# Performance work log

Measured on AMD Instinct MI355X. Metric: run time of the kernel, lower is better.

Reference implementation:

```python
import jax, jax.numpy as jnp
import numpy as np

HEADS = 8


def setup_inputs() -> dict:
    key = jax.random.key(0)
    k1, k2, k3, k4, k5, k6 = jax.random.split(key, 6)
    B, S, E = 2, 2048, 512
    D = E // HEADS
    return {
        "values": jax.random.normal(k1, (B, S, E), dtype=jnp.float32),
        "keys": jax.random.normal(k2, (B, S, E), dtype=jnp.float32),
        "queries": jax.random.normal(k3, (B, S, E), dtype=jnp.float32),
        "mask": jax.random.randint(k4, (B, 1, 1, S), 0, 2, dtype=jnp.int32),
        "W_v": jax.random.normal(k5, (D, D), dtype=jnp.float32) * (1.0 / np.sqrt(D)),
        "W_o": jax.random.normal(k6, (E, E), dtype=jnp.float32) * (1.0 / np.sqrt(E)),
        "b_o": jnp.zeros((E,), dtype=jnp.float32),
    }


def reference(values, keys, queries, mask, W_v, W_o, b_o):
    B, S, E = queries.shape
    H = HEADS
    D = E // H
    # reshape to (b, s, h, d) and apply the SAME W_v linear to v, k, q
    # (faithful to the original, which calls self.values on all three)
    v = jnp.einsum('bshd,ed->bshe', values.reshape(B, -1, H, D), W_v)
    k = jnp.einsum('bshd,ed->bshe', keys.reshape(B, -1, H, D), W_v)
    q = jnp.einsum('bshd,ed->bshe', queries.reshape(B, -1, H, D), W_v)
    # unscaled attention scores (original has no 1/sqrt(d))
    energy = jnp.einsum('bqhd,bkhd->bhqk', q, k)  # (b, h, q, k)
    energy = jnp.where(mask == 0, -jnp.inf, energy)
    attn = jax.nn.softmax(energy, axis=3)
    out = jnp.einsum('bhqk,bkhd->bqhd', attn, v)  # (b, q, h, d)
    out = out.reshape(B, S, E)
    return out @ W_o.T + b_o
```

## Files before the change

kernel.cpp:

```cpp
#include <hip/hip_runtime.h>


#define B_ 2
#define S_ 2048
#define E_ 512
#define H_ 8
#define D_ 64

#define LOG2E 1.4426950408889634f
#define KEEP_BIAS (-92.332483f)

typedef unsigned short ushort_t;
typedef __attribute__((ext_vector_type(8))) short short8;
typedef __attribute__((ext_vector_type(8))) _Float16 half8;
typedef __attribute__((ext_vector_type(4))) float f32x4;

__device__ __forceinline__ ushort_t f2bs(float x) {
    union { float f; unsigned int u; } a; a.f = x;
    unsigned int u = a.u;
    u += 0x7fffu + ((u >> 16) & 1u);
    return (ushort_t)(u >> 16);
}
__device__ __forceinline__ ushort_t f2hs(float x) {
    _Float16 h = (_Float16)x;
    ushort_t u; __builtin_memcpy(&u, &h, 2);
    return u;
}

__global__ void __launch_bounds__(256) proj_mfma(
    const float* __restrict__ quer, const float* __restrict__ keys,
    const float* __restrict__ vals, const float* __restrict__ Wv,
    const float* __restrict__ Wo,
    ushort_t* __restrict__ qf, ushort_t* __restrict__ kf,
    ushort_t* __restrict__ vt, ushort_t* __restrict__ Wob)
{
    __shared__ ushort_t As[64 * 72];
    __shared__ ushort_t Bs[64 * 72];
    const int tens = blockIdx.y;
    const int bx = blockIdx.x;
    const int t = threadIdx.x;

    if (tens == 3) {
        if (bx < 128) {
            int g = (bx * 256 + t) * 8;
            float4 f0 = *(const float4*)(Wo + g);
            float4 f1 = *(const float4*)(Wo + g + 4);
            ushort_t tmp[8] = {f2bs(f0.x), f2bs(f0.y), f2bs(f0.z), f2bs(f0.w),
                               f2bs(f1.x), f2bs(f1.y), f2bs(f1.z), f2bs(f1.w)};
            *(uint4*)&Wob[g] = *(uint4*)tmp;
        }
        return;
    }

    const float* src = tens == 0 ? quer : (tens == 1 ? keys : vals);
    const int st = bx & 31, bh = bx >> 5;
    const int b = bh >> 3, h = bh & 7;
    const int s0 = st * 64;

    {
        int e = t >> 2, dg = (t & 3) * 16;
        const float4* g = (const float4*)(Wv + e * 64 + dg);
        ushort_t tmp[16];
        #pragma unroll
        for (int q = 0; q < 4; ++q) {
            float4 f = g[q];
            tmp[q * 4 + 0] = f2hs(f.x); tmp[q * 4 + 1] = f2hs(f.y);
            tmp[q * 4 + 2] = f2hs(f.z); tmp[q * 4 + 3] = f2hs(f.w);
        }
        *(uint4*)&Bs[e * 72 + dg]     = *(uint4*)tmp;
        *(uint4*)&Bs[e * 72 + dg + 8] = *(uint4*)(tmp + 8);
    }
    {
        int row = t >> 2, cg = (t & 3) * 16;
        const float4* g = (const float4*)(src + ((size_t)b * S_ + s0 + row) * 512 + h * 64 + cg);
        ushort_t tmp[16];
        #pragma unroll
        for (int q = 0; q < 4; ++q) {
            float4 f = g[q];
            tmp[q * 4 + 0] = f2hs(f.x); tmp[q * 4 + 1] = f2hs(f.y);
            tmp[q * 4 + 2] = f2hs(f.z); tmp[q * 4 + 3] = f2hs(f.w);
        }
        *(uint4*)&As[row * 72 + cg]     = *(uint4*)tmp;
        *(uint4*)&As[row * 72 + cg + 8] = *(uint4*)(tmp + 8);
    }
    __syncthreads();

    const int w = t >> 6, lm = t & 15, quad = (t >> 4) & 3;
    f32x4 acc[4];
    #pragma unroll
    for (int nt = 0; nt < 4; ++nt) acc[nt] = (f32x4){0.f, 0.f, 0.f, 0.f};

    __builtin_amdgcn_s_setprio(1);
    #pragma unroll
    for (int kk = 0; kk < 2; ++kk) {
        half8 a = *(const half8*)&As[(w * 16 + lm) * 72 + kk * 32 + quad * 8];
        #pragma unroll
        for (int nt = 0; nt < 4; ++nt) {
            half8 bb = *(const half8*)&Bs[(nt * 16 + lm) * 72 + kk * 32 + quad * 8];
            acc[nt] = __builtin_amdgcn_mfma_f32_16x16x32_f16(a, bb, acc[nt], 0, 0, 0);
        }
    }
    __builtin_amdgcn_s_setprio(0);

    if (tens < 2) {
        ushort_t* dst = tens == 0 ? qf : kf;
        const float sc = tens == 0 ? LOG2E : 1.0f;
        #pragma unroll
        for (int nt = 0; nt < 4; ++nt) {
            #pragma unroll
            for (int r = 0; r < 4; ++r) {
                size_t addr = ((size_t)bh * S_ + s0 + w * 16 + quad * 4 + r) * 64 + nt * 16 + lm;
                dst[addr] = f2hs(acc[nt][r] * sc);
            }
        }
    } else {
        #pragma unroll
        for (int nt = 0; nt < 4; ++nt) {
            unsigned int p0 = (unsigned int)f2bs(acc[nt][0]) | ((unsigned int)f2bs(acc[nt][1]) << 16);
            unsigned int p1 = (unsigned int)f2bs(acc[nt][2]) | ((unsigned int)f2bs(acc[nt][3]) << 16);
            uint2 pk; pk.x = p0; pk.y = p1;
            size_t addr = ((size_t)bh * 64 + nt * 16 + lm) * S_ + s0 + w * 16 + quad * 4;
            *(uint2*)&vt[addr] = pk;
        }
    }
}

__global__ void __launch_bounds__(512, 4) attn_mfma(
    const ushort_t* __restrict__ qf, const ushort_t* __restrict__ kf,
    const ushort_t* __restrict__ vt, const int* __restrict__ mask,
    ushort_t* __restrict__ ctx)
{
    __shared__ ushort_t Ks[2][64 * 72];
    __shared__ ushort_t Vt[2][64 * 72];
    __shared__ ushort_t Ps[8 * 16 * 72];
    __shared__ float    mb[2][64];

    const int bx = blockIdx.x;
    const int qt = bx & 31;
    const int bh = bx >> 5;
    const int b  = bh >> 3;
    const int t  = threadIdx.x;
    const int w  = t >> 6;
    const int wq = w & 3;
    const int ws = w >> 2;
    const int lm = t & 15, quad = (t >> 4) & 3;
    const int q0 = qt * 64;
    const int wbase = w * 16 * 72;

    const int srow = t >> 3;
    const int scg  = (t & 7) * 8;
    const size_t kgbase = ((size_t)bh * S_ + srow) * 64 + scg;
    const size_t vgbase = ((size_t)bh * 64 + srow) * S_ + scg;

    half8 aq[2];
    {
        size_t qrow = ((size_t)bh * S_ + q0 + wq * 16 + lm) * 64 + quad * 8;
        aq[0] = *(const half8*)&qf[qrow];
        aq[1] = *(const half8*)&qf[qrow + 32];
    }
    short8 ones;
    #pragma unroll
    for (int j = 0; j < 8; ++j) ones[j] = (short)0x3F80;

    f32x4 acc[4];
    #pragma unroll
    for (int nt = 0; nt < 4; ++nt) acc[nt] = (f32x4){0.f, 0.f, 0.f, 0.f};
    f32x4 acc_l = (f32x4){0.f, 0.f, 0.f, 0.f};

    {
        *(uint4*)&Ks[0][srow * 72 + scg] = *(const uint4*)&kf[kgbase];
        *(uint4*)&Ks[1][srow * 72 + scg] = *(const uint4*)&kf[kgbase + 4096];
        *(uint4*)&Vt[0][srow * 72 + scg] = *(const uint4*)&vt[vgbase];
        *(uint4*)&Vt[1][srow * 72 + scg] = *(const uint4*)&vt[vgbase + 64];
        if (t < 128) mb[t >> 6][t & 63] = mask[b * S_ + t] ? KEEP_BIAS : -1e30f;
    }
    __syncthreads();

    for (int is = 0; is < S_ / 128; ++is) {
        const bool pf = (is + 1) < (S_ / 128);

        uint4 pk0, pk1, pv0, pv1; int mnx = 0;
        if (pf) {
            size_t ko = kgbase + (size_t)(2 * (is + 1)) * 4096;
            pk0 = *(const uint4*)&kf[ko];
            pk1 = *(const uint4*)&kf[ko + 4096];
            size_t vo = vgbase + (size_t)(2 * (is + 1)) * 64;
            pv0 = *(const uint4*)&vt[vo];
            pv1 = *(const uint4*)&vt[vo + 64];
            if (t < 128) mnx = mask[b * S_ + (2 * (is + 1)) * 64 + t];
        }

        const ushort_t* Kc = Ks[ws];
        const ushort_t* Vc = Vt[ws];

        #pragma unroll
        for (int nt = 0; nt < 4; ++nt) {
            f32x4 s = *(const f32x4*)&mb[ws][nt * 16 + quad * 4];
            __builtin_amdgcn_s_setprio(1);
            #pragma unroll
            for (int kk = 0; kk < 2; ++kk) {
                half8 ak = *(const half8*)&Kc[(nt * 16 + lm) * 72 + kk * 32 + quad * 8];
                s = __builtin_amdgcn_mfma_f32_16x16x32_f16(ak, aq[kk], s, 0, 0, 0);
            }
            __builtin_amdgcn_s_setprio(0);
            float p0 = __builtin_amdgcn_exp2f(s[0]);
            float p1 = __builtin_amdgcn_exp2f(s[1]);
            float p2 = __builtin_amdgcn_exp2f(s[2]);
            float p3 = __builtin_amdgcn_exp2f(s[3]);
            uint2 pkd;
            pkd.x = (unsigned int)f2bs(p0) | ((unsigned int)f2bs(p1) << 16);
            pkd.y = (unsigned int)f2bs(p2) | ((unsigned int)f2bs(p3) << 16);
            *(uint2*)&Ps[wbase + lm * 72 + nt * 16 + quad * 4] = pkd;
        }

        __builtin_amdgcn_s_setprio(1);
        #pragma unroll
        for (int kk = 0; kk < 2; ++kk) {
            short8 ap = *(const short8*)&Ps[wbase + lm * 72 + kk * 32 + quad * 8];
            #pragma unroll
            for (int nt = 0; nt < 4; ++nt) {
                short8 bv = *(const short8*)&Vc[(nt * 16 + lm) * 72 + kk * 32 + quad * 8];
                acc[nt] = __builtin_amdgcn_mfma_f32_16x16x32_bf16(ap, bv, acc[nt], 0, 0, 0);
            }
            acc_l = __builtin_amdgcn_mfma_f32_16x16x32_bf16(ap, ones, acc_l, 0, 0, 0);
        }
        __builtin_amdgcn_s_setprio(0);

        __syncthreads();
        if (pf) {
            *(uint4*)&Ks[0][srow * 72 + scg] = pk0;
            *(uint4*)&Ks[1][srow * 72 + scg] = pk1;
            *(uint4*)&Vt[0][srow * 72 + scg] = pv0;
            *(uint4*)&Vt[1][srow * 72 + scg] = pv1;
            if (t < 128) mb[t >> 6][t & 63] = mnx ? KEEP_BIAS : -1e30f;
            __syncthreads();
        }
    }

    float* cf = (float*)Ps;
    const int lane = t & 63;
    __syncthreads();
    if (ws == 1) {
        const int base = (wq * 64 + lane) * 18;
        #pragma unroll
        for (int nt = 0; nt < 4; ++nt) {
            #pragma unroll
            for (int r = 0; r < 4; r += 2) {
                float2 v2; v2.x = acc[nt][r]; v2.y = acc[nt][r + 1];
                *(float2*)&cf[base + nt * 4 + r] = v2;
            }
        }
    }
    __syncthreads();
    if (ws == 0) {
        const int base = (wq * 64 + lane) * 18;
        #pragma unroll
        for (int nt = 0; nt < 4; ++nt) {
            #pragma unroll
            for (int r = 0; r < 4; ++r) acc[nt][r] += cf[base + nt * 4 + r];
        }
    }
    __syncthreads();
    if (ws == 1) {
        const int base = (wq * 64 + lane) * 5;
        #pragma unroll
        for (int r = 0; r < 4; ++r) cf[base + r] = acc_l[r];
    }
    __syncthreads();

    if (ws == 0) {
        const int base = (wq * 64 + lane) * 5;
        #pragma unroll
        for (int r = 0; r < 4; ++r) acc_l[r] += cf[base + r];
        const int h = bh & 7;
        #pragma unroll
        for (int r = 0; r < 4; ++r) {
            float inv = 1.f / acc_l[r];
            int s = q0 + wq * 16 + quad * 4 + r;
            #pragma unroll
            for (int nt = 0; nt < 4; ++nt) {
                int d = nt * 16 + lm;
                ctx[((size_t)b * S_ + s) * E_ + h * D_ + d] = f2bs(acc[nt][r] * inv);
            }
        }
    }
}

__global__ void __launch_bounds__(512, 4) outproj_mfma(
    const ushort_t* __restrict__ ctx, const ushort_t* __restrict__ Wob,
    const float* __restrict__ bo, float* __restrict__ out)
{
    __shared__ ushort_t sm[4][64 * 72];
    const int m0 = blockIdx.x * 64, n0 = blockIdx.y * 64;
    const int t = threadIdx.x;
    const int w = t >> 6, wq = w & 3, wk = w >> 2;
    const int lm = t & 15, quad = (t >> 4) & 3;
    const int srow = t >> 3, scg = (t & 7) * 8;

    const size_t abase = (size_t)(m0 + srow) * E_ + scg;
    const size_t bbase = (size_t)(n0 + srow) * E_ + scg;

    f32x4 acc[4];
    #pragma unroll
    for (int nt = 0; nt < 4; ++nt) acc[nt] = (f32x4){0.f, 0.f, 0.f, 0.f};

    *(uint4*)&sm[0][srow * 72 + scg] = *(const uint4*)&ctx[abase];
    *(uint4*)&sm[1][srow * 72 + scg] = *(const uint4*)&ctx[abase + 256];
    *(uint4*)&sm[2][srow * 72 + scg] = *(const uint4*)&Wob[bbase];
    *(uint4*)&sm[3][srow * 72 + scg] = *(const uint4*)&Wob[bbase + 256];
    __syncthreads();

    const ushort_t* Ac = sm[wk];
    const ushort_t* Bc = sm[2 + wk];

    for (int is = 0; is < 4; ++is) {
        const bool pf = is < 3;
        uint4 pa0, pa1, pb0, pb1;
        if (pf) {
            pa0 = *(const uint4*)&ctx[abase + (size_t)(is + 1) * 64];
            pa1 = *(const uint4*)&ctx[abase + 256 + (size_t)(is + 1) * 64];
            pb0 = *(const uint4*)&Wob[bbase + (size_t)(is + 1) * 64];
            pb1 = *(const uint4*)&Wob[bbase + 256 + (size_t)(is + 1) * 64];
        }

        __builtin_amdgcn_s_setprio(1);
        #pragma unroll
        for (int kk = 0; kk < 2; ++kk) {
            short8 a = *(const short8*)&Ac[(wq * 16 + lm) * 72 + kk * 32 + quad * 8];
            #pragma unroll
            for (int nt = 0; nt < 4; ++nt) {
                short8 bb = *(const short8*)&Bc[(nt * 16 + lm) * 72 + kk * 32 + quad * 8];
                acc[nt] = __builtin_amdgcn_mfma_f32_16x16x32_bf16(a, bb, acc[nt], 0, 0, 0);
            }
        }
        __builtin_amdgcn_s_setprio(0);

        __syncthreads();
        if (pf) {
            *(uint4*)&sm[0][srow * 72 + scg] = pa0;
            *(uint4*)&sm[1][srow * 72 + scg] = pa1;
            *(uint4*)&sm[2][srow * 72 + scg] = pb0;
            *(uint4*)&sm[3][srow * 72 + scg] = pb1;
            __syncthreads();
        }
    }

    float* cf = (float*)sm;
    const int lane = t & 63;
    if (wk == 1) {
        const int base = (wq * 64 + lane) * 18;
        #pragma unroll
        for (int nt = 0; nt < 4; ++nt) {
            #pragma unroll
            for (int r = 0; r < 4; r += 2) {
                float2 v2; v2.x = acc[nt][r]; v2.y = acc[nt][r + 1];
                *(float2*)&cf[base + nt * 4 + r] = v2;
            }
        }
    }
    __syncthreads();
    if (wk == 0) {
        const int base = (wq * 64 + lane) * 18;
        #pragma unroll
        for (int nt = 0; nt < 4; ++nt) {
            float bias = bo[n0 + nt * 16 + lm];
            #pragma unroll
            for (int r = 0; r < 4; ++r) {
                int m = m0 + wq * 16 + quad * 4 + r;
                out[(size_t)m * E_ + n0 + nt * 16 + lm] =
                    acc[nt][r] + cf[base + nt * 4 + r] + bias;
            }
        }
    }
}

extern "C" void kernel_launch(void* const* d_in, const int* in_sizes, int n_in,
                              void* d_out, int out_size, void* d_ws, size_t ws_size,
                              hipStream_t stream) {
    const float* vals = (const float*)d_in[0];
    const float* keys = (const float*)d_in[1];
    const float* quer = (const float*)d_in[2];
    const int*   mask = (const int*)d_in[3];
    const float* Wv   = (const float*)d_in[4];
    const float* Wo   = (const float*)d_in[5];
    const float* bo   = (const float*)d_in[6];
    float* out = (float*)d_out;

    const size_t N = (size_t)B_ * H_ * S_ * D_;
    ushort_t* ws  = (ushort_t*)d_ws;
    ushort_t* qf  = ws;
    ushort_t* kf  = ws + N;
    ushort_t* vt  = ws + 2 * N;
    ushort_t* ctx = ws + 3 * N;
    ushort_t* Wob = ws + 4 * N;

    proj_mfma<<<dim3(B_ * H_ * (S_ / 64), 4), 256, 0, stream>>>(
        quer, keys, vals, Wv, Wo, qf, kf, vt, Wob);
    attn_mfma<<<B_ * H_ * (S_ / 64), 512, 0, stream>>>(qf, kf, vt, mask, ctx);
    outproj_mfma<<<dim3((B_ * S_) / 64, E_ / 64), 512, 0, stream>>>(ctx, Wob, bo, out);
}
```

Before: 124.6 us.

## Load V fragments directly from global, double-buffer K in LDS, swizzle block order

The attention kernel stops staging V^T through shared memory and has each lane load its MFMA B-operand fragments straight from global memory every iteration. K and the mask bias are now double-buffered in LDS, which cuts the loop to one barrier per iteration instead of two. The block index is remapped so neighbouring blocks spread across heads. The aim is to reduce LDS traffic and synchronisation, in exchange for less-coalesced global V loads whose latency sits on the critical path and for more LDS used by the K double buffer.

New measurement: 158.7 us. 27.4% more time.

```diff
diff --git a/kernel.cpp b/kernel.cpp
--- a/kernel.cpp
+++ b/kernel.cpp
@@ -130,12 +130,12 @@
     const ushort_t* __restrict__ vt, const int* __restrict__ mask,
     ushort_t* __restrict__ ctx)
 {
-    __shared__ ushort_t Ks[2][64 * 72];
-    __shared__ ushort_t Vt[2][64 * 72];
+    __shared__ ushort_t Ks[2][2][64 * 72];
     __shared__ ushort_t Ps[8 * 16 * 72];
-    __shared__ float    mb[2][64];
-
-    const int bx = blockIdx.x;
+    __shared__ float    mb[2][2][64];
+
+    const int bx0 = blockIdx.x;
+    const int bx = (bx0 & 7) * 64 + (bx0 >> 3);
     const int qt = bx & 31;
     const int bh = bx >> 5;
     const int b  = bh >> 3;
@@ -150,7 +150,8 @@
     const int srow = t >> 3;
     const int scg  = (t & 7) * 8;
     const size_t kgbase = ((size_t)bh * S_ + srow) * 64 + scg;
-    const size_t vgbase = ((size_t)bh * 64 + srow) * S_ + scg;
+
+    const ushort_t* vB = vt + ((size_t)bh * 64 + lm) * S_ + quad * 8;
 
     half8 aq[2];
     {
@@ -168,34 +169,39 @@
     f32x4 acc_l = (f32x4){0.f, 0.f, 0.f, 0.f};
 
     {
-        *(uint4*)&Ks[0][srow * 72 + scg] = *(const uint4*)&kf[kgbase];
-        *(uint4*)&Ks[1][srow * 72 + scg] = *(const uint4*)&kf[kgbase + 4096];
-        *(uint4*)&Vt[0][srow * 72 + scg] = *(const uint4*)&vt[vgbase];
-        *(uint4*)&Vt[1][srow * 72 + scg] = *(const uint4*)&vt[vgbase + 64];
-        if (t < 128) mb[t >> 6][t & 63] = mask[b * S_ + t] ? KEEP_BIAS : -1e30f;
-    }
-    __syncthreads();
-
-    for (int is = 0; is < S_ / 128; ++is) {
-        const bool pf = (is + 1) < (S_ / 128);
-
-        uint4 pk0, pk1, pv0, pv1; int mnx = 0;
+        *(uint4*)&Ks[0][0][srow * 72 + scg] = *(const uint4*)&kf[kgbase];
+        *(uint4*)&Ks[0][1][srow * 72 + scg] = *(const uint4*)&kf[kgbase + 4096];
+        if (t < 128) mb[0][t >> 6][t & 63] = mask[b * S_ + t] ? KEEP_BIAS : -1e30f;
+    }
+    __syncthreads();
+
+    for (int is = 0; is < 16; ++is) {
+        const int cbuf = is & 1, nbuf = cbuf ^ 1;
+        const bool pf = is < 15;
+
+        uint4 pk0, pk1; int mnx = 0;
         if (pf) {
             size_t ko = kgbase + (size_t)(2 * (is + 1)) * 4096;
             pk0 = *(const uint4*)&kf[ko];
             pk1 = *(const uint4*)&kf[ko + 4096];
-            size_t vo = vgbase + (size_t)(2 * (is + 1)) * 64;
-            pv0 = *(const uint4*)&vt[vo];
-            pv1 = *(const uint4*)&vt[vo + 64];
-            if (t < 128) mnx = mask[b * S_ + (2 * (is + 1)) * 64 + t];
-        }
-
-        const ushort_t* Kc = Ks[ws];
-        const ushort_t* Vc = Vt[ws];
-
-        #pragma unroll
-        for (int nt = 0; nt < 4; ++nt) {
-            f32x4 s = *(const f32x4*)&mb[ws][nt * 16 + quad * 4];
+            if (t < 128) mnx = mask[b * S_ + (is + 1) * 128 + t];
+        }
+
+        const size_t vtile = (size_t)(2 * is + ws) * 64;
+        short8 bv00 = *(const short8*)&vB[(size_t)0 * 16 * S_ + vtile];
+        short8 bv01 = *(const short8*)&vB[(size_t)0 * 16 * S_ + vtile + 32];
+        short8 bv10 = *(const short8*)&vB[(size_t)1 * 16 * S_ + vtile];
+        short8 bv11 = *(const short8*)&vB[(size_t)1 * 16 * S_ + vtile + 32];
+        short8 bv20 = *(const short8*)&vB[(size_t)2 * 16 * S_ + vtile];
+        short8 bv21 = *(const short8*)&vB[(size_t)2 * 16 * S_ + vtile + 32];
+        short8 bv30 = *(const short8*)&vB[(size_t)3 * 16 * S_ + vtile];
+        short8 bv31 = *(const short8*)&vB[(size_t)3 * 16 * S_ + vtile + 32];
+
+        const ushort_t* Kc = Ks[cbuf][ws];
+
+        #pragma unroll
+        for (int nt = 0; nt < 4; ++nt) {
+            f32x4 s = *(const f32x4*)&mb[cbuf][ws][nt * 16 + quad * 4];
             __builtin_amdgcn_s_setprio(1);
             #pragma unroll
             for (int kk = 0; kk < 2; ++kk) {
@@ -214,32 +220,32 @@
         }
 
         __builtin_amdgcn_s_setprio(1);
-        #pragma unroll
-        for (int kk = 0; kk < 2; ++kk) {
-            short8 ap = *(const short8*)&Ps[wbase + lm * 72 + kk * 32 + quad * 8];
-            #pragma unroll
-            for (int nt = 0; nt < 4; ++nt) {
-                short8 bv = *(const short8*)&Vc[(nt * 16 + lm) * 72 + kk * 32 + quad * 8];
-                acc[nt] = __builtin_amdgcn_mfma_f32_16x16x32_bf16(ap, bv, acc[nt], 0, 0, 0);
-            }
-            acc_l = __builtin_amdgcn_mfma_f32_16x16x32_bf16(ap, ones, acc_l, 0, 0, 0);
+        {
+            short8 ap0 = *(const short8*)&Ps[wbase + lm * 72 + quad * 8];
+            acc[0] = __builtin_amdgcn_mfma_f32_16x16x32_bf16(ap0, bv00, acc[0], 0, 0, 0);
+            acc[1] = __builtin_amdgcn_mfma_f32_16x16x32_bf16(ap0, bv10, acc[1], 0, 0, 0);
+            acc[2] = __builtin_amdgcn_mfma_f32_16x16x32_bf16(ap0, bv20, acc[2], 0, 0, 0);
+            acc[3] = __builtin_amdgcn_mfma_f32_16x16x32_bf16(ap0, bv30, acc[3], 0, 0, 0);
+            acc_l  = __builtin_amdgcn_mfma_f32_16x16x32_bf16(ap0, ones, acc_l, 0, 0, 0);
+            short8 ap1 = *(const short8*)&Ps[wbase + lm * 72 + 32 + quad * 8];
+            acc[0] = __builtin_amdgcn_mfma_f32_16x16x32_bf16(ap1, bv01, acc[0], 0, 0, 0);
+            acc[1] = __builtin_amdgcn_mfma_f32_16x16x32_bf16(ap1, bv11, acc[1], 0, 0, 0);
+            acc[2] = __builtin_amdgcn_mfma_f32_16x16x32_bf16(ap1, bv21, acc[2], 0, 0, 0);
+            acc[3] = __builtin_amdgcn_mfma_f32_16x16x32_bf16(ap1, bv31, acc[3], 0, 0, 0);
+            acc_l  = __builtin_amdgcn_mfma_f32_16x16x32_bf16(ap1, ones, acc_l, 0, 0, 0);
         }
         __builtin_amdgcn_s_setprio(0);
 
+        if (pf) {
+            *(uint4*)&Ks[nbuf][0][srow * 72 + scg] = pk0;
+            *(uint4*)&Ks[nbuf][1][srow * 72 + scg] = pk1;
+            if (t < 128) mb[nbuf][t >> 6][t & 63] = mnx ? KEEP_BIAS : -1e30f;
+        }
         __syncthreads();
-        if (pf) {
-            *(uint4*)&Ks[0][srow * 72 + scg] = pk0;
-            *(uint4*)&Ks[1][srow * 72 + scg] = pk1;
-            *(uint4*)&Vt[0][srow * 72 + scg] = pv0;
-            *(uint4*)&Vt[1][srow * 72 + scg] = pv1;
-            if (t < 128) mb[t >> 6][t & 63] = mnx ? KEEP_BIAS : -1e30f;
-            __syncthreads();
-        }
     }
 
     float* cf = (float*)Ps;
     const int lane = t & 63;
-    __syncthreads();
     if (ws == 1) {
         const int base = (wq * 64 + lane) * 18;
         #pragma unroll
```
